# Performance work log

Hardware: AMD Instinct MI355X
Metric: run time of the kernel (lower is better)

The kernel has to match this reference:

```python
import jax, jax.numpy as jnp
import numpy as np

B, TX, TZ, DX, DZ, DATT, DMID, H, DOUT = 8, 1024, 1024, 1024, 1024, 64, 64, 16, 1024


def setup_inputs() -> dict:
    key = jax.random.key(0)
    ks = jax.random.split(key, 10)
    s = 0.02
    return {
        "x": jax.random.normal(ks[0], (B, TX, DX), jnp.float32),
        "z": jax.random.normal(ks[1], (B, TZ, DZ), jnp.float32),
        "Wq": jax.random.normal(ks[2], (H, DX, DATT), jnp.float32) * s,
        "bq": jax.random.normal(ks[3], (H, DATT), jnp.float32) * s,
        "Wk": jax.random.normal(ks[4], (H, DZ, DATT), jnp.float32) * s,
        "bk": jax.random.normal(ks[5], (H, DATT), jnp.float32) * s,
        "Wv": jax.random.normal(ks[6], (H, DZ, DMID), jnp.float32) * s,
        "bv": jax.random.normal(ks[7], (H, DMID), jnp.float32) * s,
        "Wp": jax.random.normal(ks[8], (H * DMID, DOUT), jnp.float32) * s,
        "bp": jax.random.normal(ks[9], (DOUT,), jnp.float32) * s,
        "mask": jnp.tril(jnp.ones((TX, TZ), dtype=bool)),  # causal
    }


def reference(x, z, Wq, bq, Wk, bk, Wv, bv, Wp, bp, mask):
    # Per-head projections (heads batched via stacked weights). bhxe = batch, head, x-pos, feat
    Q = jnp.einsum('bxd,hde->bhxe', x, Wq) + bq[None, :, None, :]
    K = jnp.einsum('bzd,hde->bhze', z, Wk) + bk[None, :, None, :]
    V = jnp.einsum('bzd,hde->bhze', z, Wv) + bv[None, :, None, :]
    # Scores, mask (set ~mask to -inf), then scale by 1/sqrt(Datt) (as original: mask before scale)
    S = jnp.einsum('bhxe,bhze->bhxz', Q, K)
    S = jnp.where(mask[None, None, :, :], S, -jnp.inf) * (1.0 / jnp.sqrt(jnp.asarray(DATT, S.dtype)))
    A = jax.nn.softmax(S, axis=-1)
    y = jnp.einsum('bhxz,bhze->bhxe', A, V)          # [B, H, Tx, Dmid]
    y_concat = y.transpose(0, 2, 1, 3).reshape(B, TX, H * DMID)  # concat heads
    return y_concat @ Wp + bp
```

## Files before the change

### kernel.cpp

```cpp
#include <hip/hip_runtime.h>
#include <stdint.h>


typedef float    f32x4  __attribute__((ext_vector_type(4)));
typedef __bf16   bf16x8 __attribute__((ext_vector_type(8)));
typedef unsigned short u16x4 __attribute__((ext_vector_type(4)));
typedef unsigned short u16x8 __attribute__((ext_vector_type(8)));

#define MASKNEG (-3.0e38f)
#define QSCALE_F (0.125f * 1.4426950408889634f)

__device__ __forceinline__ unsigned short f2bf(float f) {
  unsigned int u = __float_as_uint(f);
  u += 0x7fffu + ((u >> 16) & 1u);
  return (unsigned short)(u >> 16);
}

__device__ __forceinline__ unsigned short f2bf_hw(float f) {
  __bf16 h = (__bf16)f;
  return *(unsigned short*)&h;
}

__device__ __forceinline__ void gload16(const void* g, void* s) {
  const __attribute__((address_space(1))) unsigned int* gp =
      (const __attribute__((address_space(1))) unsigned int*)(uintptr_t)g;
  __attribute__((address_space(3))) unsigned int* lp =
      (__attribute__((address_space(3))) unsigned int*)(unsigned int)(uintptr_t)s;
  __builtin_amdgcn_global_load_lds(gp, lp, 16, 0, 0);
}

__device__ __forceinline__ f32x4 mfma16(bf16x8 a, bf16x8 b, f32x4 c) {
  return __builtin_amdgcn_mfma_f32_16x16x32_bf16(a, b, c, 0, 0, 0);
}

__global__ __launch_bounds__(256) void k_prep(const float* __restrict__ x,
                                              const float* __restrict__ z,
                                              unsigned short* __restrict__ out,
                                              const float* __restrict__ Wq,
                                              const float* __restrict__ Wk,
                                              const float* __restrict__ Wv,
                                              const float* __restrict__ Wp,
                                              unsigned short* __restrict__ Oq,
                                              unsigned short* __restrict__ Ok,
                                              unsigned short* __restrict__ Ov,
                                              unsigned short* __restrict__ Op) {
  __shared__ float tile[64][65];
  const int bid = blockIdx.x;
  const int t = threadIdx.x;

  if (bid < 2048) {
    int i = bid * 256 + t;
    const int stride = 2048 * 256;
    for (; i < 2097152; i += stride) {
      const float* in = (i < 1048576) ? (x + (size_t)i * 8) : (z + (size_t)(i - 1048576) * 8);
      const f32x4* p = (const f32x4*)in;
      f32x4 a = p[0], b = p[1];
      u16x8 o;
      o[0] = f2bf(a[0]); o[1] = f2bf(a[1]); o[2] = f2bf(a[2]); o[3] = f2bf(a[3]);
      o[4] = f2bf(b[0]); o[5] = f2bf(b[1]); o[6] = f2bf(b[2]); o[7] = f2bf(b[3]);
      *(u16x8*)(out + (size_t)i * 8) = o;
    }
    return;
  }

  const int pid = bid - 2048;
  const int zid = pid >> 8;
  const int bx = (pid >> 4) & 15;
  const int by = pid & 15;

  if (zid < 3) {
    const float* W = zid == 0 ? Wq : (zid == 1 ? Wk : Wv);
    unsigned short* O = zid == 0 ? Oq : (zid == 1 ? Ok : Ov);
    const int h = bx, d0 = by * 64;
    const int ee = t & 63, r0 = t >> 6;
#pragma unroll
    for (int dd = r0; dd < 64; dd += 4)
      tile[dd][ee] = W[(h * 1024 + d0 + dd) * 64 + ee];
    __syncthreads();
    const int d = t & 63, e0 = t >> 6;
#pragma unroll
    for (int e = e0; e < 64; e += 4)
      O[(h * 64 + e) * 1024 + d0 + d] = f2bf(tile[d][e]);
  } else {
    const int k0 = bx * 64, n0 = by * 64;
    const int nn = t & 63, r0 = t >> 6;
#pragma unroll
    for (int kk = r0; kk < 64; kk += 4)
      tile[kk][nn] = Wp[(k0 + kk) * 1024 + n0 + nn];
    __syncthreads();
    const int kk = t & 63, e0 = t >> 6;
#pragma unroll
    for (int n2 = e0; n2 < 64; n2 += 4)
      Op[(n0 + n2) * 1024 + k0 + kk] = f2bf(tile[kk][n2]);
  }
}

__device__ __forceinline__ void gemm_body(const unsigned short* __restrict__ A,
                                          const unsigned short* __restrict__ Bt,
                                          const float* __restrict__ bias,
                                          void* __restrict__ outp,
                                          int mode, float oscale,
                                          int brow, int bcol,
                                          unsigned short* As, unsigned short* Bs) {
  const int tid = threadIdx.x;
  const int l = tid & 63, w = tid >> 6;
  const int lrow = l & 15, lk = l >> 4;
  const int wr = (w >> 1) * 128, wc = (w & 1) * 64;

  const int arow = tid >> 2;
  const int asrc = ((tid & 3) ^ ((arow >> 1) & 3)) * 8;
  const unsigned short* ag0 = A + (size_t)(brow + arow) * 1024 + asrc;
  const unsigned short* bg0 = Bt + (size_t)(bcol + arow) * 1024 + asrc;

  int aoff[8], boff[4];
#pragma unroll
  for (int m = 0; m < 8; m++) {
    int row = wr + m * 16 + lrow;
    aoff[m] = row * 64 + ((lk ^ ((row >> 1) & 3)) << 4);
  }
#pragma unroll
  for (int n = 0; n < 4; n++) {
    int col = wc + n * 16 + lrow;
    boff[n] = col * 64 + ((lk ^ ((col >> 1) & 3)) << 4);
  }

  f32x4 acc[8][4];
#pragma unroll
  for (int n = 0; n < 4; n++) {
    float bv = bias[bcol + wc + n * 16 + lrow];
#pragma unroll
    for (int m = 0; m < 8; m++) acc[m][n] = (f32x4){bv, bv, bv, bv};
  }

#define STAGE_G(kt, slot)                                                  \
  {                                                                        \
    char* asb = (char*)As + (slot) * 16384 + w * 1024;                     \
    char* bsb = (char*)Bs + (slot) * 8192 + w * 1024;                      \
    gload16(ag0 + (kt) * 32,          asb);                                \
    gload16(ag0 + (kt) * 32 + 65536,  asb + 4096);                         \
    gload16(ag0 + (kt) * 32 + 131072, asb + 8192);                         \
    gload16(ag0 + (kt) * 32 + 196608, asb + 12288);                        \
    gload16(bg0 + (kt) * 32,          bsb);                                \
    gload16(bg0 + (kt) * 32 + 65536,  bsb + 4096);                         \
  }

  STAGE_G(0, 0)
  asm volatile("s_waitcnt vmcnt(0)" ::: "memory");
  __builtin_amdgcn_s_barrier();
  __builtin_amdgcn_sched_barrier(0);

#pragma unroll 1
  for (int kt = 0; kt < 32; kt++) {
    const int cur = kt & 1;
    if (kt < 31) STAGE_G(kt + 1, cur ^ 1)
    const char* ab = (const char*)As + cur * 16384;
    const char* bb = (const char*)Bs + cur * 8192;
    bf16x8 bfr[4];
#pragma unroll
    for (int n = 0; n < 4; n++) bfr[n] = *(const bf16x8*)(bb + boff[n]);
#pragma unroll
    for (int m = 0; m < 8; m++) {
      bf16x8 af = *(const bf16x8*)(ab + aoff[m]);
#pragma unroll
      for (int n = 0; n < 4; n++)
        acc[m][n] = mfma16(af, bfr[n], acc[m][n]);
    }
    if (kt < 31) {
      asm volatile("s_waitcnt vmcnt(0)" ::: "memory");
      __builtin_amdgcn_s_barrier();
      __builtin_amdgcn_sched_barrier(0);
    }
  }
#undef STAGE_G

  if (mode == 0) {
    unsigned short* C = (unsigned short*)outp;
#pragma unroll
    for (int m = 0; m < 8; m++) {
      int r = brow + wr + m * 16 + 4 * lk;
#pragma unroll
      for (int n = 0; n < 4; n++) {
        int c = bcol + wc + n * 16 + lrow;
        unsigned short* p = C + ((r >> 10) * 16 + (c >> 6)) * 65536 + (r & 1023) * 64 + (c & 63);
#pragma unroll
        for (int j = 0; j < 4; j++) p[j * 64] = f2bf(acc[m][n][j] * oscale);
      }
    }
  } else if (mode == 2) {
    unsigned short* C = (unsigned short*)outp;
#pragma unroll
    for (int m = 0; m < 8; m++) {
      int r = brow + wr + m * 16 + 4 * lk;
#pragma unroll
      for (int n = 0; n < 4; n++) {
        int c = bcol + wc + n * 16 + lrow;
        u16x4 o;
#pragma unroll
        for (int j = 0; j < 4; j++) o[j] = f2bf(acc[m][n][j]);
        *(u16x4*)(C + ((r >> 10) * 16 + (c >> 6)) * 65536 + (c & 63) * 1024 + (r & 1023)) = o;
      }
    }
  } else {
    float* C = (float*)outp;
#pragma unroll
    for (int m = 0; m < 8; m++) {
      int r = brow + wr + m * 16 + 4 * lk;
#pragma unroll
      for (int n = 0; n < 4; n++) {
        int c = bcol + wc + n * 16 + lrow;
#pragma unroll
        for (int j = 0; j < 4; j++) C[(r + j) * 1024 + c] = acc[m][n][j];
      }
    }
  }
}

__global__ __launch_bounds__(256, 3) void k_gemm_qkv(const unsigned short* __restrict__ Xb,
                                                     const unsigned short* __restrict__ Zb,
                                                     const unsigned short* __restrict__ Wqkv,
                                                     const float* __restrict__ bq,
                                                     const float* __restrict__ bk,
                                                     const float* __restrict__ bv,
                                                     unsigned short* __restrict__ Qp,
                                                     unsigned short* __restrict__ Kp,
                                                     unsigned short* __restrict__ Vtp) {
  __shared__ unsigned short As[16384];
  __shared__ unsigned short Bs[8192];
  const int brow = blockIdx.x * 256;
  const int cg = blockIdx.y;
  const int seg = cg >> 3;
  const int bcol = (cg & 7) * 128;
  const unsigned short* A = (seg == 0) ? Xb : Zb;
  const unsigned short* Bt = Wqkv + (size_t)seg * 1048576;
  const float* bias = (seg == 0) ? bq : (seg == 1 ? bk : bv);
  void* outp = (seg == 0) ? (void*)Qp : (seg == 1 ? (void*)Kp : (void*)Vtp);
  const int mode = (seg == 2) ? 2 : 0;
  const float oscale = (seg == 0) ? QSCALE_F : 1.0f;
  gemm_body(A, Bt, bias, outp, mode, oscale, brow, bcol, As, Bs);
}

__global__ __launch_bounds__(256, 3) void k_gemm(const unsigned short* __restrict__ A,
                                                 const unsigned short* __restrict__ Bt,
                                                 const float* __restrict__ bias,
                                                 void* __restrict__ outp,
                                                 int mode, float oscale) {
  __shared__ unsigned short As[16384];
  __shared__ unsigned short Bs[8192];
  gemm_body(A, Bt, bias, outp, mode, oscale, blockIdx.x * 256, blockIdx.y * 128, As, Bs);
}

__global__ __launch_bounds__(256, 2) void k_attn(const unsigned short* __restrict__ Qh,
                                                 const unsigned short* __restrict__ Kh,
                                                 const unsigned short* __restrict__ Vth,
                                                 unsigned short* __restrict__ Y) {
  __shared__ unsigned short Ks[16384];
  __shared__ unsigned short Vs[16384];
  __shared__ unsigned short Ps[8192];

  const int tid = threadIdx.x, l = tid & 63, w = tid >> 6;
  const int lrow = l & 15, lk = l >> 4;
  const int bh = blockIdx.x;
  const int pp = blockIdx.y;

  const unsigned short* Qb = Qh + bh * 65536;
  const unsigned short* Kb = Kh + bh * 65536;
  const unsigned short* Vb = Vth + bh * 65536;

  bf16x8 ones;
#pragma unroll
  for (int j = 0; j < 8; j++) ones[j] = (__bf16)1.0f;

  const int krl = l >> 3;
  const int kgp = l & 7;
  const unsigned short* kgsrc = Kb + (w * 32 + krl) * 64 + ((kgp ^ krl) * 8);
  const int vrl = l >> 4;
  const int vgp = l & 15;
  const int vr0 = w * 16 + 0 * 4 + vrl;
  const int vr1 = w * 16 + 1 * 4 + vrl;
  const int vr2 = w * 16 + 2 * 4 + vrl;
  const int vr3 = w * 16 + 3 * 4 + vrl;
  const int voff0 = vr0 * 1024 + ((vgp ^ (vr0 & 15)) * 8);
  const int voff1 = vr1 * 1024 + ((vgp ^ (vr1 & 15)) * 8);
  const int voff2 = vr2 * 1024 + ((vgp ^ (vr2 & 15)) * 8);
  const int voff3 = vr3 * 1024 + ((vgp ^ (vr3 & 15)) * 8);

  char* pw = (char*)Ps + w * 4096;

  const int b = bh >> 4, h = bh & 15;

#pragma unroll 1
  for (int hp = 0; hp < 2; hp++) {
    const int qi = hp == 0 ? (7 - pp) : pp;
    const int qw = qi * 128 + w * 32;
    const int qmax = qw + 31;

    bf16x8 qf[2][2];
#pragma unroll
    for (int qn = 0; qn < 2; qn++) {
      const unsigned short* qp = Qb + (qw + qn * 16 + lrow) * 64 + lk * 8;
      qf[qn][0] = *(const bf16x8*)qp;
      qf[qn][1] = *(const bf16x8*)(qp + 32);
    }

    float mm[2];
    f32x4 lsum[2], yacc[2][4];
#pragma unroll
    for (int qn = 0; qn < 2; qn++) {
      mm[qn] = MASKNEG;
      lsum[qn] = (f32x4){0.f, 0.f, 0.f, 0.f};
#pragma unroll
      for (int ef = 0; ef < 4; ef++) yacc[qn][ef] = (f32x4){0.f, 0.f, 0.f, 0.f};
    }

    const int nt = qi + 1;

    {
      char* kb = (char*)Ks + w * 4096;
      char* vb2 = (char*)Vs + w * 4096;
      gload16(kgsrc + 0,    kb);
      gload16(kgsrc + 512,  kb + 1024);
      gload16(kgsrc + 1024, kb + 2048);
      gload16(kgsrc + 1536, kb + 3072);
      gload16(Vb + voff0, vb2);
      gload16(Vb + voff1, vb2 + 1024);
      gload16(Vb + voff2, vb2 + 2048);
      gload16(Vb + voff3, vb2 + 3072);
    }
    __syncthreads();

#pragma unroll 1
    for (int t = 0; t < nt; t++) {
      const int z0 = t * 128;
      const int cur = t & 1;
      if (t < nt - 1) {
        const int zn = (t + 1) * 128;
        char* kb = (char*)Ks + (cur ^ 1) * 16384 + w * 4096;
        char* vb2 = (char*)Vs + (cur ^ 1) * 16384 + w * 4096;
        const unsigned short* kgt = kgsrc + zn * 64;
        gload16(kgt + 0,    kb);
        gload16(kgt + 512,  kb + 1024);
        gload16(kgt + 1024, kb + 2048);
        gload16(kgt + 1536, kb + 3072);
        gload16(Vb + voff0 + zn, vb2);
        gload16(Vb + voff1 + zn, vb2 + 1024);
        gload16(Vb + voff2 + zn, vb2 + 2048);
        gload16(Vb + voff3 + zn, vb2 + 3072);
      }

      if (z0 <= qmax) {
        const char* kbase = (const char*)Ks + cur * 16384;
        const char* vbase = (const char*)Vs + cur * 16384;

        f32x4 s[2][8];
#pragma unroll
        for (int qn = 0; qn < 2; qn++)
#pragma unroll
          for (int zf = 0; zf < 8; zf++) s[qn][zf] = (f32x4){0.f, 0.f, 0.f, 0.f};
#pragma unroll
        for (int zf = 0; zf < 8; zf++) {
          int zr = zf * 16 + lrow;
#pragma unroll
          for (int kf = 0; kf < 2; kf++) {
            bf16x8 kfr = *(const bf16x8*)(kbase + zr * 128 + (((kf * 4 + lk) ^ (zr & 7)) << 4));
            s[0][zf] = mfma16(kfr, qf[0][kf], s[0][zf]);
            s[1][zf] = mfma16(kfr, qf[1][kf], s[1][zf]);
          }
        }

        if (z0 + 127 > qw) {
#pragma unroll
          for (int qn = 0; qn < 2; qn++) {
            int qg = qw + qn * 16 + lrow;
#pragma unroll
            for (int zf = 0; zf < 8; zf++) {
              int zb = z0 + zf * 16 + 4 * lk;
#pragma unroll
              for (int j = 0; j < 4; j++)
                if (zb + j > qg) s[qn][zf][j] = MASKNEG;
            }
          }
        }

#pragma unroll
        for (int qn = 0; qn < 2; qn++) {
          f32x4 r4 = s[qn][0];
#pragma unroll
          for (int zf = 1; zf < 8; zf++)
#pragma unroll
            for (int j = 0; j < 4; j++) r4[j] = fmaxf(r4[j], s[qn][zf][j]);
          float rm = fmaxf(fmaxf(r4[0], r4[1]), fmaxf(r4[2], r4[3]));
          rm = fmaxf(rm, __shfl_xor(rm, 16));
          rm = fmaxf(rm, __shfl_xor(rm, 32));

          if (__any(rm > mm[qn] + 8.f)) {
            float mn = fmaxf(mm[qn], rm);
            float a = __builtin_amdgcn_exp2f(mm[qn] - mn);
            mm[qn] = mn;
            f32x4 av;
#pragma unroll
            for (int j = 0; j < 4; j++)
              av[j] = __shfl(a, (l & 48) | (lk * 4 + j));
            lsum[qn] *= av;
#pragma unroll
            for (int ef = 0; ef < 4; ef++) yacc[qn][ef] *= av;
          }
          float mk = mm[qn];
#pragma unroll
          for (int zf = 0; zf < 8; zf++)
#pragma unroll
            for (int j = 0; j < 4; j++)
              s[qn][zf][j] = __builtin_amdgcn_exp2f(s[qn][zf][j] - mk);
        }

#pragma unroll
        for (int hf = 0; hf < 2; hf++) {
          if (z0 + hf * 64 <= qmax) {
#pragma unroll
            for (int qn = 0; qn < 2; qn++) {
              int q = qn * 16 + lrow;
              char* rowp = pw + q * 128;
#pragma unroll
              for (int zf2 = 0; zf2 < 4; zf2++) {
                int zfg = hf * 4 + zf2;
                u16x4 o;
#pragma unroll
                for (int j = 0; j < 4; j++) o[j] = f2bf_hw(s[qn][zfg][j]);
                int g = zf2 * 2 + (lk >> 1);
                *(u16x4*)(rowp + ((g ^ (q & 7)) << 4) + (lk & 1) * 8) = o;
              }
            }

            asm volatile("s_waitcnt lgkmcnt(0)" ::: "memory");
            __builtin_amdgcn_sched_barrier(0);

            bf16x8 pf[2][2];
#pragma unroll
            for (int qn = 0; qn < 2; qn++)
#pragma unroll
              for (int kf = 0; kf < 2; kf++)
                pf[qn][kf] = *(const bf16x8*)(pw + (qn * 16 + lrow) * 128 + (((kf * 4 + lk) ^ (lrow & 7)) << 4));

#pragma unroll
            for (int qn = 0; qn < 2; qn++)
#pragma unroll
              for (int kf = 0; kf < 2; kf++)
                lsum[qn] = mfma16(pf[qn][kf], ones, lsum[qn]);

#pragma unroll
            for (int ef = 0; ef < 4; ef++) {
              int er = ef * 16 + lrow;
#pragma unroll
              for (int kf = 0; kf < 2; kf++) {
                int g = hf * 8 + kf * 4 + lk;
                bf16x8 vf = *(const bf16x8*)(vbase + er * 256 + ((g ^ (er & 15)) << 4));
                yacc[0][ef] = mfma16(pf[0][kf], vf, yacc[0][ef]);
                yacc[1][ef] = mfma16(pf[1][kf], vf, yacc[1][ef]);
              }
            }
          }
        }
      }

      __syncthreads();
    }

#pragma unroll
    for (int qn = 0; qn < 2; qn++) {
      f32x4 rinv;
#pragma unroll
      for (int j = 0; j < 4; j++) rinv[j] = 1.0f / lsum[qn][j];
#pragma unroll
      for (int ef = 0; ef < 4; ef++) {
        int col = h * 64 + ef * 16 + lrow;
#pragma unroll
        for (int j = 0; j < 4; j++) {
          int x = qw + qn * 16 + lk * 4 + j;
          Y[(b * 1024 + x) * 1024 + col] = f2bf_hw(yacc[qn][ef][j] * rinv[j]);
        }
      }
    }
  }
}

extern "C" void kernel_launch(void* const* d_in, const int* in_sizes, int n_in,
                              void* d_out, int out_size, void* d_ws, size_t ws_size,
                              hipStream_t stream) {
  const float* x  = (const float*)d_in[0];
  const float* z  = (const float*)d_in[1];
  const float* Wq = (const float*)d_in[2];
  const float* bq = (const float*)d_in[3];
  const float* Wk = (const float*)d_in[4];
  const float* bk = (const float*)d_in[5];
  const float* Wv = (const float*)d_in[6];
  const float* bv = (const float*)d_in[7];
  const float* Wp = (const float*)d_in[8];
  const float* bp = (const float*)d_in[9];
  (void)in_sizes; (void)n_in; (void)out_size; (void)ws_size;

  char* ws = (char*)d_ws;
  unsigned short* Xb  = (unsigned short*)(ws + 0);
  unsigned short* Zb  = (unsigned short*)(ws + 16777216);
  unsigned short* Wqt = (unsigned short*)(ws + 33554432);
  unsigned short* Wkt = (unsigned short*)(ws + 35651584);
  unsigned short* Wvt = (unsigned short*)(ws + 37748736);
  unsigned short* Wpt = (unsigned short*)(ws + 39845888);
  unsigned short* Qp  = (unsigned short*)(ws + 41943040);
  unsigned short* Kp  = (unsigned short*)(ws + 58720256);
  unsigned short* Vtp = (unsigned short*)(ws + 75497472);

  k_prep<<<dim3(3072), dim3(256), 0, stream>>>(x, z, Xb, Wq, Wk, Wv, Wp, Wqt, Wkt, Wvt, Wpt);

  k_gemm_qkv<<<dim3(32, 24), dim3(256), 0, stream>>>(Xb, Zb, Wqt, bq, bk, bv, Qp, Kp, Vtp);

  k_attn<<<dim3(128, 4), dim3(256), 0, stream>>>(Qp, Kp, Vtp, Xb );

  k_gemm<<<dim3(32, 8), dim3(256), 0, stream>>>(Xb, Wpt, bp, d_out, 3, 1.0f);
}
```

Before: 143.0 us.

## Process both paired query blocks in one pass over shared K/V tiles

The attention kernel previously handled its two causal-paired query blocks one after the other, streaming K/V tiles from global memory into LDS twice. Now both query blocks keep their own accumulators and run against each K/V tile loaded once, over the longer block's tile range. This removes the duplicate K/V loads for the shorter block and halves the barrier-synchronised tile iterations. In exchange, roughly twice as many accumulator registers are live, which may lower occupancy or cause spills under launch_bounds(256,2).

```diff
diff --git a/kernel.cpp b/kernel.cpp
--- a/kernel.cpp
+++ b/kernel.cpp
@@ -249,6 +249,123 @@
   gemm_body(A, Bt, bias, outp, mode, oscale, blockIdx.x * 256, blockIdx.y * 128, As, Bs);
 }
 
+__device__ __forceinline__ void attn_tile(const char* kbase, const char* vbase, char* pw,
+                                          int l, int lrow, int lk, int z0, int qw, int qmax,
+                                          const bf16x8 (&qf)[2][2], float (&mm)[2],
+                                          f32x4 (&lsum)[2], f32x4 (&yacc)[2][4],
+                                          bf16x8 ones) {
+  if (z0 > qmax) return;
+
+  f32x4 s[2][8];
+#pragma unroll
+  for (int qn = 0; qn < 2; qn++)
+#pragma unroll
+    for (int zf = 0; zf < 8; zf++) s[qn][zf] = (f32x4){0.f, 0.f, 0.f, 0.f};
+#pragma unroll
+  for (int zf = 0; zf < 8; zf++) {
+    int zr = zf * 16 + lrow;
+#pragma unroll
+    for (int kf = 0; kf < 2; kf++) {
+      bf16x8 kfr = *(const bf16x8*)(kbase + zr * 128 + (((kf * 4 + lk) ^ (zr & 7)) << 4));
+      s[0][zf] = mfma16(kfr, qf[0][kf], s[0][zf]);
+      s[1][zf] = mfma16(kfr, qf[1][kf], s[1][zf]);
+    }
+  }
+
+  if (z0 + 127 > qw) {
+#pragma unroll
+    for (int qn = 0; qn < 2; qn++) {
+      int qg = qw + qn * 16 + lrow;
+#pragma unroll
+      for (int zf = 0; zf < 8; zf++) {
+        int zb = z0 + zf * 16 + 4 * lk;
+#pragma unroll
+        for (int j = 0; j < 4; j++)
+          if (zb + j > qg) s[qn][zf][j] = MASKNEG;
+      }
+    }
+  }
+
+#pragma unroll
+  for (int qn = 0; qn < 2; qn++) {
+    f32x4 r4 = s[qn][0];
+#pragma unroll
+    for (int zf = 1; zf < 8; zf++)
+#pragma unroll
+      for (int j = 0; j < 4; j++) r4[j] = fmaxf(r4[j], s[qn][zf][j]);
+    float rm = fmaxf(fmaxf(r4[0], r4[1]), fmaxf(r4[2], r4[3]));
+    rm = fmaxf(rm, __shfl_xor(rm, 16));
+    rm = fmaxf(rm, __shfl_xor(rm, 32));
+
+    if (__any(rm > mm[qn] + 8.f)) {
+      float mn = fmaxf(mm[qn], rm);
+      float a = __builtin_amdgcn_exp2f(mm[qn] - mn);
+      mm[qn] = mn;
+      f32x4 av;
+#pragma unroll
+      for (int j = 0; j < 4; j++)
+        av[j] = __shfl(a, (l & 48) | (lk * 4 + j));
+      lsum[qn] *= av;
+#pragma unroll
+      for (int ef = 0; ef < 4; ef++) yacc[qn][ef] *= av;
+    }
+    float mk = mm[qn];
+#pragma unroll
+    for (int zf = 0; zf < 8; zf++)
+#pragma unroll
+      for (int j = 0; j < 4; j++)
+        s[qn][zf][j] = __builtin_amdgcn_exp2f(s[qn][zf][j] - mk);
+  }
+
+#pragma unroll
+  for (int hf = 0; hf < 2; hf++) {
+    if (z0 + hf * 64 <= qmax) {
+#pragma unroll
+      for (int qn = 0; qn < 2; qn++) {
+        int q = qn * 16 + lrow;
+        char* rowp = pw + q * 128;
+#pragma unroll
+        for (int zf2 = 0; zf2 < 4; zf2++) {
+          int zfg = hf * 4 + zf2;
+          u16x4 o;
+#pragma unroll
+          for (int j = 0; j < 4; j++) o[j] = f2bf_hw(s[qn][zfg][j]);
+          int g = zf2 * 2 + (lk >> 1);
+          *(u16x4*)(rowp + ((g ^ (q & 7)) << 4) + (lk & 1) * 8) = o;
+        }
+      }
+
+      asm volatile("s_waitcnt lgkmcnt(0)" ::: "memory");
+      __builtin_amdgcn_sched_barrier(0);
+
+      bf16x8 pf[2][2];
+#pragma unroll
+      for (int qn = 0; qn < 2; qn++)
+#pragma unroll
+        for (int kf = 0; kf < 2; kf++)
+          pf[qn][kf] = *(const bf16x8*)(pw + (qn * 16 + lrow) * 128 + (((kf * 4 + lk) ^ (lrow & 7)) << 4));
+
+#pragma unroll
+      for (int qn = 0; qn < 2; qn++)
+#pragma unroll
+        for (int kf = 0; kf < 2; kf++)
+          lsum[qn] = mfma16(pf[qn][kf], ones, lsum[qn]);
+
+#pragma unroll
+      for (int ef = 0; ef < 4; ef++) {
+        int er = ef * 16 + lrow;
+#pragma unroll
+        for (int kf = 0; kf < 2; kf++) {
+          int g = hf * 8 + kf * 4 + lk;
+          bf16x8 vf = *(const bf16x8*)(vbase + er * 256 + ((g ^ (er & 15)) << 4));
+          yacc[0][ef] = mfma16(pf[0][kf], vf, yacc[0][ef]);
+          yacc[1][ef] = mfma16(pf[1][kf], vf, yacc[1][ef]);
+        }
+      }
+    }
+  }
+}
+
 __global__ __launch_bounds__(256, 2) void k_attn(const unsigned short* __restrict__ Qh,
                                                  const unsigned short* __restrict__ Kh,
                                                  const unsigned short* __restrict__ Vth,
@@ -288,195 +405,105 @@
 
   const int b = bh >> 4, h = bh & 15;
 
+  const int qwA = (7 - pp) * 128 + w * 32, qmaxA = qwA + 31;
+  const int qwB = pp * 128 + w * 32,       qmaxB = qwB + 31;
+
+  bf16x8 qfA[2][2], qfB[2][2];
+#pragma unroll
+  for (int qn = 0; qn < 2; qn++) {
+    const unsigned short* qpA = Qb + (qwA + qn * 16 + lrow) * 64 + lk * 8;
+    qfA[qn][0] = *(const bf16x8*)qpA;
+    qfA[qn][1] = *(const bf16x8*)(qpA + 32);
+    const unsigned short* qpB = Qb + (qwB + qn * 16 + lrow) * 64 + lk * 8;
+    qfB[qn][0] = *(const bf16x8*)qpB;
+    qfB[qn][1] = *(const bf16x8*)(qpB + 32);
+  }
+
+  float mmA[2], mmB[2];
+  f32x4 lsumA[2], lsumB[2], yaccA[2][4], yaccB[2][4];
+#pragma unroll
+  for (int qn = 0; qn < 2; qn++) {
+    mmA[qn] = MASKNEG; mmB[qn] = MASKNEG;
+    lsumA[qn] = (f32x4){0.f, 0.f, 0.f, 0.f};
+    lsumB[qn] = (f32x4){0.f, 0.f, 0.f, 0.f};
+#pragma unroll
+    for (int ef = 0; ef < 4; ef++) {
+      yaccA[qn][ef] = (f32x4){0.f, 0.f, 0.f, 0.f};
+      yaccB[qn][ef] = (f32x4){0.f, 0.f, 0.f, 0.f};
+    }
+  }
+
+  const int nt = 8 - pp;
+
+  {
+    char* kb = (char*)Ks + w * 4096;
+    char* vb2 = (char*)Vs + w * 4096;
+    gload16(kgsrc + 0,    kb);
+    gload16(kgsrc + 512,  kb + 1024);
+    gload16(kgsrc + 1024, kb + 2048);
+    gload16(kgsrc + 1536, kb + 3072);
+    gload16(Vb + voff0, vb2);
+    gload16(Vb + voff1, vb2 + 1024);
+    gload16(Vb + voff2, vb2 + 2048);
+    gload16(Vb + voff3, vb2 + 3072);
+  }
+  __syncthreads();
+
 #pragma unroll 1
-  for (int hp = 0; hp < 2; hp++) {
-    const int qi = hp == 0 ? (7 - pp) : pp;
-    const int qw = qi * 128 + w * 32;
-    const int qmax = qw + 31;
-
-    bf16x8 qf[2][2];
-#pragma unroll
-    for (int qn = 0; qn < 2; qn++) {
-      const unsigned short* qp = Qb + (qw + qn * 16 + lrow) * 64 + lk * 8;
-      qf[qn][0] = *(const bf16x8*)qp;
-      qf[qn][1] = *(const bf16x8*)(qp + 32);
-    }
-
-    float mm[2];
-    f32x4 lsum[2], yacc[2][4];
-#pragma unroll
-    for (int qn = 0; qn < 2; qn++) {
-      mm[qn] = MASKNEG;
-      lsum[qn] = (f32x4){0.f, 0.f, 0.f, 0.f};
-#pragma unroll
-      for (int ef = 0; ef < 4; ef++) yacc[qn][ef] = (f32x4){0.f, 0.f, 0.f, 0.f};
-    }
-
-    const int nt = qi + 1;
-
-    {
-      char* kb = (char*)Ks + w * 4096;
-      char* vb2 = (char*)Vs + w * 4096;
-      gload16(kgsrc + 0,    kb);
-      gload16(kgsrc + 512,  kb + 1024);
-      gload16(kgsrc + 1024, kb + 2048);
-      gload16(kgsrc + 1536, kb + 3072);
-      gload16(Vb + voff0, vb2);
-      gload16(Vb + voff1, vb2 + 1024);
-      gload16(Vb + voff2, vb2 + 2048);
-      gload16(Vb + voff3, vb2 + 3072);
-    }
+  for (int t = 0; t < nt; t++) {
+    const int z0 = t * 128;
+    const int cur = t & 1;
+    if (t < nt - 1) {
+      const int zn = (t + 1) * 128;
+      char* kb = (char*)Ks + (cur ^ 1) * 16384 + w * 4096;
+      char* vb2 = (char*)Vs + (cur ^ 1) * 16384 + w * 4096;
+      const unsigned short* kgt = kgsrc + zn * 64;
+      gload16(kgt + 0,    kb);
+      gload16(kgt + 512,  kb + 1024);
+      gload16(kgt + 1024, kb + 2048);
+      gload16(kgt + 1536, kb + 3072);
+      gload16(Vb + voff0 + zn, vb2);
+      gload16(Vb + voff1 + zn, vb2 + 1024);
+      gload16(Vb + voff2 + zn, vb2 + 2048);
+      gload16(Vb + voff3 + zn, vb2 + 3072);
+    }
+
+    const char* kbase = (const char*)Ks + cur * 16384;
+    const char* vbase = (const char*)Vs + cur * 16384;
+
+    attn_tile(kbase, vbase, pw, l, lrow, lk, z0, qwA, qmaxA, qfA, mmA, lsumA, yaccA, ones);
+    attn_tile(kbase, vbase, pw, l, lrow, lk, z0, qwB, qmaxB, qfB, mmB, lsumB, yaccB, ones);
+
     __syncthreads();
-
-#pragma unroll 1
-    for (int t = 0; t < nt; t++) {
-      const int z0 = t * 128;
-      const int cur = t & 1;
-      if (t < nt - 1) {
-        const int zn = (t + 1) * 128;
-        char* kb = (char*)Ks + (cur ^ 1) * 16384 + w * 4096;
-        char* vb2 = (char*)Vs + (cur ^ 1) * 16384 + w * 4096;
-        const unsigned short* kgt = kgsrc + zn * 64;
-        gload16(kgt + 0,    kb);
-        gload16(kgt + 512,  kb + 1024);
-        gload16(kgt + 1024, kb + 2048);
-        gload16(kgt + 1536, kb + 3072);
-        gload16(Vb + voff0 + zn, vb2);
-        gload16(Vb + voff1 + zn, vb2 + 1024);
-        gload16(Vb + voff2 + zn, vb2 + 2048);
-        gload16(Vb + voff3 + zn, vb2 + 3072);
-      }
-
-      if (z0 <= qmax) {
-        const char* kbase = (const char*)Ks + cur * 16384;
-        const char* vbase = (const char*)Vs + cur * 16384;
-
-        f32x4 s[2][8];
-#pragma unroll
-        for (int qn = 0; qn < 2; qn++)
-#pragma unroll
-          for (int zf = 0; zf < 8; zf++) s[qn][zf] = (f32x4){0.f, 0.f, 0.f, 0.f};
-#pragma unroll
-        for (int zf = 0; zf < 8; zf++) {
-          int zr = zf * 16 + lrow;
-#pragma unroll
-          for (int kf = 0; kf < 2; kf++) {
-            bf16x8 kfr = *(const bf16x8*)(kbase + zr * 128 + (((kf * 4 + lk) ^ (zr & 7)) << 4));
-            s[0][zf] = mfma16(kfr, qf[0][kf], s[0][zf]);
-            s[1][zf] = mfma16(kfr, qf[1][kf], s[1][zf]);
-          }
-        }
-
-        if (z0 + 127 > qw) {
-#pragma unroll
-          for (int qn = 0; qn < 2; qn++) {
-            int qg = qw + qn * 16 + lrow;
-#pragma unroll
-            for (int zf = 0; zf < 8; zf++) {
-              int zb = z0 + zf * 16 + 4 * lk;
-#pragma unroll
-              for (int j = 0; j < 4; j++)
-                if (zb + j > qg) s[qn][zf][j] = MASKNEG;
-            }
-          }
-        }
-
-#pragma unroll
-        for (int qn = 0; qn < 2; qn++) {
-          f32x4 r4 = s[qn][0];
-#pragma unroll
-          for (int zf = 1; zf < 8; zf++)
-#pragma unroll
-            for (int j = 0; j < 4; j++) r4[j] = fmaxf(r4[j], s[qn][zf][j]);
-          float rm = fmaxf(fmaxf(r4[0], r4[1]), fmaxf(r4[2], r4[3]));
-          rm = fmaxf(rm, __shfl_xor(rm, 16));
-          rm = fmaxf(rm, __shfl_xor(rm, 32));
-
-          if (__any(rm > mm[qn] + 8.f)) {
-            float mn = fmaxf(mm[qn], rm);
-            float a = __builtin_amdgcn_exp2f(mm[qn] - mn);
-            mm[qn] = mn;
-            f32x4 av;
-#pragma unroll
-            for (int j = 0; j < 4; j++)
-              av[j] = __shfl(a, (l & 48) | (lk * 4 + j));
-            lsum[qn] *= av;
-#pragma unroll
-            for (int ef = 0; ef < 4; ef++) yacc[qn][ef] *= av;
-          }
-          float mk = mm[qn];
-#pragma unroll
-          for (int zf = 0; zf < 8; zf++)
-#pragma unroll
-            for (int j = 0; j < 4; j++)
-              s[qn][zf][j] = __builtin_amdgcn_exp2f(s[qn][zf][j] - mk);
-        }
-
-#pragma unroll
-        for (int hf = 0; hf < 2; hf++) {
-          if (z0 + hf * 64 <= qmax) {
-#pragma unroll
-            for (int qn = 0; qn < 2; qn++) {
-              int q = qn * 16 + lrow;
-              char* rowp = pw + q * 128;
-#pragma unroll
-              for (int zf2 = 0; zf2 < 4; zf2++) {
-                int zfg = hf * 4 + zf2;
-                u16x4 o;
-#pragma unroll
-                for (int j = 0; j < 4; j++) o[j] = f2bf_hw(s[qn][zfg][j]);
-                int g = zf2 * 2 + (lk >> 1);
-                *(u16x4*)(rowp + ((g ^ (q & 7)) << 4) + (lk & 1) * 8) = o;
-              }
-            }
-
-            asm volatile("s_waitcnt lgkmcnt(0)" ::: "memory");
-            __builtin_amdgcn_sched_barrier(0);
-
-            bf16x8 pf[2][2];
-#pragma unroll
-            for (int qn = 0; qn < 2; qn++)
-#pragma unroll
-              for (int kf = 0; kf < 2; kf++)
-                pf[qn][kf] = *(const bf16x8*)(pw + (qn * 16 + lrow) * 128 + (((kf * 4 + lk) ^ (lrow & 7)) << 4));
-
-#pragma unroll
-            for (int qn = 0; qn < 2; qn++)
-#pragma unroll
-              for (int kf = 0; kf < 2; kf++)
-                lsum[qn] = mfma16(pf[qn][kf], ones, lsum[qn]);
-
-#pragma unroll
-            for (int ef = 0; ef < 4; ef++) {
-              int er = ef * 16 + lrow;
-#pragma unroll
-              for (int kf = 0; kf < 2; kf++) {
-                int g = hf * 8 + kf * 4 + lk;
-                bf16x8 vf = *(const bf16x8*)(vbase + er * 256 + ((g ^ (er & 15)) << 4));
-                yacc[0][ef] = mfma16(pf[0][kf], vf, yacc[0][ef]);
-                yacc[1][ef] = mfma16(pf[1][kf], vf, yacc[1][ef]);
-              }
-            }
-          }
-        }
-      }
-
-      __syncthreads();
-    }
-
-#pragma unroll
-    for (int qn = 0; qn < 2; qn++) {
-      f32x4 rinv;
-#pragma unroll
-      for (int j = 0; j < 4; j++) rinv[j] = 1.0f / lsum[qn][j];
-#pragma unroll
-      for (int ef = 0; ef < 4; ef++) {
-        int col = h * 64 + ef * 16 + lrow;
-#pragma unroll
-        for (int j = 0; j < 4; j++) {
-          int x = qw + qn * 16 + lk * 4 + j;
-          Y[(b * 1024 + x) * 1024 + col] = f2bf_hw(yacc[qn][ef][j] * rinv[j]);
-        }
+  }
+
+#pragma unroll
+  for (int qn = 0; qn < 2; qn++) {
+    f32x4 rinv;
+#pragma unroll
+    for (int j = 0; j < 4; j++) rinv[j] = 1.0f / lsumA[qn][j];
+#pragma unroll
+    for (int ef = 0; ef < 4; ef++) {
+      int col = h * 64 + ef * 16 + lrow;
+#pragma unroll
+      for (int j = 0; j < 4; j++) {
+        int xq = qwA + qn * 16 + lk * 4 + j;
+        Y[(b * 1024 + xq) * 1024 + col] = f2bf_hw(yaccA[qn][ef][j] * rinv[j]);
+      }
+    }
+  }
+#pragma unroll
+  for (int qn = 0; qn < 2; qn++) {
+    f32x4 rinv;
+#pragma unroll
+    for (int j = 0; j < 4; j++) rinv[j] = 1.0f / lsumB[qn][j];
+#pragma unroll
+    for (int ef = 0; ef < 4; ef++) {
+      int col = h * 64 + ef * 16 + lrow;
+#pragma unroll
+      for (int j = 0; j < 4; j++) {
+        int xq = qwB + qn * 16 + lk * 4 + j;
+        Y[(b * 1024 + xq) * 1024 + col] = f2bf_hw(yaccB[qn][ef][j] * rinv[j]);
       }
     }
   }
```

Result: no change. 143.0 us (+0.1%).
